# Optimization experiments

Hardware: AMD Instinct MI355X
Metric: run time of the kernel (lower is better)

Reference implementation:

```python
import jax, jax.numpy as jnp
import numpy as np

B, N, E, D, OUT, L = 4, 10000, 160000, 128, 64, 4
NEG = 0.01  # LeakyReLU slope

def lrelu(x):
    return jnp.where(x > 0, x, NEG * x)

def setup_inputs() -> dict:
    key = jax.random.key(0)
    ks = jax.random.split(key, 20)
    s = 0.05
    inp = {
        "x": jax.random.normal(ks[0], (B, N * 3), dtype=jnp.float32),
        "edge_index": jax.random.randint(ks[1], (2, E), 0, N, dtype=jnp.int32),
        # f0: Linear(3, D)
        "w0": jax.random.normal(ks[2], (3, D), dtype=jnp.float32) * s,
        "b0": jax.random.normal(ks[3], (D,), dtype=jnp.float32) * s,
        # per-layer params stacked on leading L axis
        "ew1": jax.random.normal(ks[4], (L, 2 * D + 1, D), dtype=jnp.float32) * s,
        "eb1": jax.random.normal(ks[5], (L, D), dtype=jnp.float32) * s,
        "ew2": jax.random.normal(ks[6], (L, D, D), dtype=jnp.float32) * s,
        "eb2": jax.random.normal(ks[7], (L, D), dtype=jnp.float32) * s,
        "cw": jax.random.normal(ks[8], (L, D, 1), dtype=jnp.float32) * s,
        "cb": jax.random.normal(ks[9], (L, 1), dtype=jnp.float32) * s,
        "nw1": jax.random.normal(ks[10], (L, 2 * D, D), dtype=jnp.float32) * s,
        "nb1": jax.random.normal(ks[11], (L, D), dtype=jnp.float32) * s,
        "nw2": jax.random.normal(ks[12], (L, D, D), dtype=jnp.float32) * s,
        "nb2": jax.random.normal(ks[13], (L, D), dtype=jnp.float32) * s,
        # project: Linear(D, OUT)
        "wp": jax.random.normal(ks[14], (D, OUT), dtype=jnp.float32) * s,
        "bp": jax.random.normal(ks[15], (OUT,), dtype=jnp.float32) * s,
    }
    return inp

def reference(x, edge_index, w0, b0, ew1, eb1, ew2, eb2, cw, cb, nw1, nb1, nw2, nb2, wp, bp):
    b = x.shape[0]
    n = x.shape[1] // 3
    pos = x.reshape(b, n, 3)            # coordinates [B,N,3]
    h = lrelu(pos @ w0 + b0)            # node features [B,N,D]
    row, col = edge_index[0], edge_index[1]
    # per-node in-edge counts (same for all layers/batches); scatter_mean -> 0 for empty nodes
    cnt = jnp.zeros((n,), x.dtype).at[col].add(1.0)
    denom = jnp.maximum(cnt, 1.0)[None, :, None]
    for i in range(L):
        rel = pos[:, row] - pos[:, col]                          # [B,E,3]
        dist_sq = jnp.sum(rel * rel, axis=-1, keepdims=True)     # [B,E,1]
        edge_in = jnp.concatenate([h[:, row], h[:, col], dist_sq], axis=-1)  # [B,E,2D+1]
        msg = lrelu(lrelu(edge_in @ ew1[i] + eb1[i]) @ ew2[i] + eb2[i])       # [B,E,D]
        aggr = jnp.zeros((b, n, msg.shape[-1]), msg.dtype).at[:, col].add(msg) / denom  # scatter_mean
        coord_update = jnp.tanh(aggr @ cw[i] + cb[i])            # [B,N,1]
        pos = pos + coord_update * 0.1
        node_in = jnp.concatenate([h, aggr], axis=-1)            # [B,N,2D]
        h = h + lrelu(lrelu(node_in @ nw1[i] + nb1[i]) @ nw2[i] + nb2[i])
    return lrelu(h.mean(axis=1) @ wp + bp)                       # [B,OUT]
```

## Files before the change

kernel.cpp:

```cpp
#include <hip/hip_runtime.h>
#include <hip/hip_bf16.h>
#include <math.h>

#define BB   4
#define NN   10000
#define NP   10112
#define NB16 (NP / 16)
#define EE   160000
#define DD   128
#define OUTD 64
#define LL   4
#define NEGS 0.01f
#define MSTR 136
#define RSH  68

typedef __attribute__((ext_vector_type(8))) short   short8;
typedef __attribute__((ext_vector_type(4))) float   floatx4;

__device__ __forceinline__ float lrelu(float x) { return fmaxf(x, NEGS * x); }
__device__ __forceinline__ ushort f2bf(float x) {
    uint u = __builtin_bit_cast(uint, x);
    return (ushort)((u + 0x7FFFu + ((u >> 16) & 1u)) >> 16);
}
__device__ __forceinline__ float bf2f(ushort u) {
    uint v = ((uint)u) << 16;
    return __builtin_bit_cast(float, v);
}

__global__ void k_cvtw(const float* __restrict__ src, ushort* __restrict__ dst,
                       int rowpitch, int nks) {
    int tid = blockIdx.x * 256 + threadIdx.x;
    if (tid >= LL * nks * 512) return;
    int lane = tid & 63;
    int nt   = (tid >> 6) & 7;
    int ks   = (tid >> 9) % nks;
    int l    = tid / (nks * 512);
    int quad = lane >> 4, l16 = lane & 15;
    int n = nt * 16 + l16;
    const float* s = src + (size_t)l * rowpitch * DD;
    ushort* d = dst + (size_t)tid * 8;
    #pragma unroll
    for (int j = 0; j < 8; ++j)
        d[j] = f2bf(s[(size_t)(ks * 32 + quad * 8 + j) * DD + n]);
}

__global__ void k_h0(const float* __restrict__ x, const float* __restrict__ w0,
                     const float* __restrict__ b0, float* __restrict__ hp,
                     ushort* __restrict__ hb) {
    int idx = blockIdx.x * 256 + threadIdx.x;
    if (idx >= BB * NP * DD) return;
    int tile = idx >> 11, in = idx & 2047;
    int b = tile / NB16, g16 = tile % NB16;
    int nt = in >> 8, lane = (in >> 2) & 63, r = in & 3;
    int quad = lane >> 4, l16 = lane & 15;
    int n = g16 * 16 + quad * 4 + r;
    int d = nt * 16 + l16;
    float v = 0.0f;
    if (n < NN) {
        const float* p = x + ((size_t)b * NN + n) * 3;
        v = lrelu(b0[d] + p[0] * w0[d] + p[1] * w0[DD + d] + p[2] * w0[2 * DD + d]);
    }
    hp[idx] = v;
    hb[((size_t)b * NP + n) * DD + d] = f2bf(v);
}

__global__ void k_count(const int* __restrict__ col, float* __restrict__ cnt,
                        int* __restrict__ ecnt) {
    int e = blockIdx.x * blockDim.x + threadIdx.x;
    if (e < EE) {
        int c = col[e];
        atomicAdd(&cnt[c], 1.0f);
        atomicAdd(&ecnt[c], 1);
    }
}

__global__ __launch_bounds__(256) void k_scan(const int* __restrict__ ecnt,
                                              int* __restrict__ cursor) {
    __shared__ int s_sum[256];
    int t = threadIdx.x;
    int base = t * 40;
    int s = 0;
    for (int i = 0; i < 40; ++i) {
        int n = base + i;
        if (n < NN) s += ecnt[n];
    }
    s_sum[t] = s;
    __syncthreads();
    if (t == 0) {
        int a = 0;
        for (int i = 0; i < 256; ++i) { int v = s_sum[i]; s_sum[i] = a; a += v; }
    }
    __syncthreads();
    int a = s_sum[t];
    for (int i = 0; i < 40; ++i) {
        int n = base + i;
        if (n < NN) { cursor[n] = a; a += ecnt[n]; }
    }
}

__global__ void k_place(const int* __restrict__ row, const int* __restrict__ col,
                        int* __restrict__ cursor,
                        int* __restrict__ rowS, int* __restrict__ colS) {
    int e = blockIdx.x * blockDim.x + threadIdx.x;
    if (e >= EE) return;
    int c = col[e];
    int p = atomicAdd(&cursor[c], 1);
    rowS[p] = row[e];
    colS[p] = c;
}

__global__ __launch_bounds__(256) void k_pq(
    const ushort* __restrict__ hb, const ushort* __restrict__ wtf,
    const ushort* __restrict__ wmf, const float* __restrict__ b1,
    ushort* __restrict__ P, ushort* __restrict__ Q)
{
    __shared__ __align__(16) ushort s_out[64 * MSTR];
    const int b = blockIdx.y, n0 = blockIdx.x * 64, t = threadIdx.x;
    const int w = t >> 6, lane = t & 63, quad = lane >> 4, l16 = lane & 15;
    const int rw = w * 16;
    const int nw = n0 + rw;

    const ushort* hptr = hb + ((size_t)b * NP + nw + l16) * DD;
    float b1r[8];
    #pragma unroll
    for (int nt = 0; nt < 8; ++nt) b1r[nt] = b1[nt * 16 + l16];

    const short8* wt = (const short8*)wtf;
    const short8* wm = (const short8*)wmf;

    #pragma unroll
    for (int pass = 0; pass < 2; ++pass) {
        floatx4 ap[8];
        #pragma unroll
        for (int nt = 0; nt < 8; ++nt)
            #pragma unroll
            for (int r = 0; r < 4; ++r) ap[nt][r] = pass ? b1r[nt] : 0.0f;
        const short8* wv = pass ? wm : wt;
        #pragma unroll
        for (int ks = 0; ks < 4; ++ks) {
            short8 bf[8];
            #pragma unroll
            for (int nt = 0; nt < 8; ++nt) bf[nt] = wv[(ks * 8 + nt) * 64 + lane];
            short8 af = *(const short8*)(hptr + ks * 32 + quad * 8);
            #pragma unroll
            for (int nt = 0; nt < 8; ++nt)
                ap[nt] = __builtin_amdgcn_mfma_f32_16x16x32_bf16(af, bf[nt], ap[nt], 0, 0, 0);
        }
        #pragma unroll
        for (int nt = 0; nt < 8; ++nt)
            #pragma unroll
            for (int r = 0; r < 4; ++r)
                s_out[(rw + quad * 4 + r) * MSTR + nt * 16 + l16] = f2bf(ap[nt][r]);
        ushort* dst = pass ? Q : P;
        #pragma unroll
        for (int i = 0; i < 4; ++i) {
            int row = rw + i * 4 + quad;
            short8 v = *(const short8*)&s_out[row * MSTR + l16 * 8];
            *(short8*)(dst + ((size_t)b * NP + n0 + row) * DD + l16 * 8) = v;
        }
    }
}

__global__ __launch_bounds__(256, 4) void k_edge(
    const float* __restrict__ pos,
    const ushort* __restrict__ P, const ushort* __restrict__ Q,
    const int* __restrict__ rowS, const int* __restrict__ colS,
    const float* __restrict__ w1last,
    const ushort* __restrict__ w2f, const float* __restrict__ b2,
    float* __restrict__ aggr)
{
    __shared__ int    s_row[128];
    __shared__ int    s_col[128];
    __shared__ float  s_ds[128];
    __shared__ __align__(16) ushort s_red[128 * RSH];

    const int g    = blockIdx.x;
    const int b    = (g >> 1) & 3;
    const int tile = (g >> 3) * 2 + (g & 1);
    const int e0   = tile * 128;
    const int t    = threadIdx.x;
    const int w    = t >> 6, lane = t & 63;
    const int quad = lane >> 4, l16 = lane & 15;

    if (t < 128) {
        int e = e0 + t;
        int r = rowS[e], c = colS[e];
        s_row[t] = r;
        s_col[t] = c;
        const float* pr = pos + ((size_t)b * NN + r) * 3;
        const float* pc = pos + ((size_t)b * NN + c) * 3;
        float dx = pr[0] - pc[0], dy = pr[1] - pc[1], dz = pr[2] - pc[2];
        s_ds[t] = dx * dx + dy * dy + dz * dz;
    }
    __syncthreads();

    const int ew = w * 32;
    const ushort* pp[2];
    const ushort* qp[2];
    float dsv[2];
    #pragma unroll
    for (int mt = 0; mt < 2; ++mt) {
        int el = ew + mt * 16 + l16;
        pp[mt]  = P + ((size_t)b * NP + s_row[el]) * DD;
        qp[mt]  = Q + ((size_t)b * NP + s_col[el]) * DD;
        dsv[mt] = s_ds[el];
    }

    short8 pf[2][4], qf[2][4];
    #pragma unroll
    for (int ks = 0; ks < 4; ++ks) {
        const int koff = ks * 32 + quad * 8;
        #pragma unroll
        for (int mt = 0; mt < 2; ++mt) {
            pf[mt][ks] = *(const short8*)(pp[mt] + koff);
            qf[mt][ks] = *(const short8*)(qp[mt] + koff);
        }
    }

    short8 mid[2][4];
    #pragma unroll
    for (int ks = 0; ks < 4; ++ks) {
        const int koff = ks * 32 + quad * 8;
        floatx4 wl0 = *(const floatx4*)(w1last + koff);
        floatx4 wl1 = *(const floatx4*)(w1last + koff + 4);
        #pragma unroll
        for (int mt = 0; mt < 2; ++mt) {
            #pragma unroll
            for (int j = 0; j < 4; ++j) {
                float v = bf2f((ushort)pf[mt][ks][j]) + bf2f((ushort)qf[mt][ks][j]) + dsv[mt] * wl0[j];
                mid[mt][ks][j] = (short)f2bf(lrelu(v));
            }
            #pragma unroll
            for (int j = 0; j < 4; ++j) {
                float v = bf2f((ushort)pf[mt][ks][4 + j]) + bf2f((ushort)qf[mt][ks][4 + j]) + dsv[mt] * wl1[j];
                mid[mt][ks][4 + j] = (short)f2bf(lrelu(v));
            }
        }
    }

    float b2r[8];
    #pragma unroll
    for (int nt = 0; nt < 8; ++nt) b2r[nt] = b2[nt * 16 + l16];

    const short8* w2v = (const short8*)w2f;
    #pragma unroll
    for (int ph = 0; ph < 2; ++ph) {
        floatx4 acc[2][4];
        #pragma unroll
        for (int mt = 0; mt < 2; ++mt)
            #pragma unroll
            for (int ntl = 0; ntl < 4; ++ntl)
                #pragma unroll
                for (int r = 0; r < 4; ++r) acc[mt][ntl][r] = b2r[ph * 4 + ntl];

        #pragma unroll
        for (int ks = 0; ks < 4; ++ks) {
            short8 bf[4];
            #pragma unroll
            for (int ntl = 0; ntl < 4; ++ntl)
                bf[ntl] = w2v[(ks * 8 + ph * 4 + ntl) * 64 + lane];
            #pragma unroll
            for (int mt = 0; mt < 2; ++mt)
                #pragma unroll
                for (int ntl = 0; ntl < 4; ++ntl)
                    acc[mt][ntl] = __builtin_amdgcn_mfma_f32_16x16x32_bf16(mid[mt][ks], bf[ntl], acc[mt][ntl], 0, 0, 0);
        }

        #pragma unroll
        for (int mt = 0; mt < 2; ++mt)
            #pragma unroll
            for (int ntl = 0; ntl < 4; ++ntl)
                #pragma unroll
                for (int r = 0; r < 4; ++r)
                    s_red[(ew + mt * 16 + quad * 4 + r) * RSH + ntl * 16 + l16] =
                        f2bf(lrelu(acc[mt][ntl][r]));

        const int d = ph * 64 + lane;
        float run = 0.0f;
        int prev = s_col[ew];
        for (int r = 0; r < 32; ++r) {
            int cid = s_col[ew + r];
            float v = bf2f(s_red[(ew + r) * RSH + lane]);
            if (cid != prev) {
                atomicAdd(&aggr[((size_t)b * NP + prev) * DD + d], run);
                run = 0.0f;
                prev = cid;
            }
            run += v;
        }
        atomicAdd(&aggr[((size_t)b * NP + prev) * DD + d], run);
    }
}

__global__ __launch_bounds__(256) void k_node(
    ushort* hb, float* aggr, const float* __restrict__ cnt,
    const float* __restrict__ cw, const float* __restrict__ cb,
    const ushort* __restrict__ w1f, const float* __restrict__ b1,
    const ushort* __restrict__ w2f, const float* __restrict__ b2,
    float* hp, float* __restrict__ pos,
    int do_pq,
    const ushort* __restrict__ wtn, const ushort* __restrict__ wmn,
    const float* __restrict__ b1n,
    ushort* __restrict__ P, ushort* __restrict__ Q)
{
    __shared__ __align__(16) ushort s_mid[64 * MSTR];
    __shared__ __align__(16) ushort s_out[64 * MSTR];

    const int g    = blockIdx.x;
    const int b    = (g >> 1) & 3;
    const int tile = (g >> 3) * 2 + (g & 1);
    const int n0   = tile * 64;
    const int t    = threadIdx.x;
    const int w    = t >> 6, lane = t & 63;
    const int quad = lane >> 4, l16 = lane & 15;
    const int rw   = w * 16;
    const int nw   = n0 + rw;

    const ushort* hptr = hb + ((size_t)b * NP + nw + l16) * DD;
    float* aptr = aggr + ((size_t)b * NP + nw + l16) * DD;
    float inv = 0.0f;
    {
        int node = nw + l16;
        if (node < NN) { float dn = cnt[node]; inv = 1.0f / fmaxf(dn, 1.0f); }
    }
    float b1r[8], b2r[8];
    #pragma unroll
    for (int nt = 0; nt < 8; ++nt) {
        int d = nt * 16 + l16;
        b1r[nt] = b1[d]; b2r[nt] = b2[d];
    }

    floatx4 acc[8];
    #pragma unroll
    for (int nt = 0; nt < 8; ++nt)
        #pragma unroll
        for (int r = 0; r < 4; ++r) acc[nt][r] = b1r[nt];

    float cwacc = 0.0f;
    const floatx4 zero4 = {0.0f, 0.0f, 0.0f, 0.0f};
    const short8* w1v = (const short8*)w1f;
    #pragma unroll
    for (int ks = 0; ks < 8; ++ks) {
        short8 bf[8];
        #pragma unroll
        for (int nt = 0; nt < 8; ++nt) bf[nt] = w1v[(ks * 8 + nt) * 64 + lane];
        const int koff = (ks & 3) * 32 + quad * 8;
        if (ks < 4) {
            short8 af = *(const short8*)(hptr + koff);
            #pragma unroll
            for (int nt = 0; nt < 8; ++nt)
                acc[nt] = __builtin_amdgcn_mfma_f32_16x16x32_bf16(af, bf[nt], acc[nt], 0, 0, 0);
        } else {
            floatx4 cw0 = *(const floatx4*)(cw + koff);
            floatx4 cw1 = *(const floatx4*)(cw + koff + 4);
            floatx4 a0 = *(const floatx4*)(aptr + koff);
            floatx4 a1 = *(const floatx4*)(aptr + koff + 4);
            *(floatx4*)(aptr + koff)     = zero4;
            *(floatx4*)(aptr + koff + 4) = zero4;
            short8 af;
            #pragma unroll
            for (int j = 0; j < 4; ++j) {
                float v = a0[j] * inv;
                af[j] = (short)f2bf(v);
                cwacc += v * cw0[j];
            }
            #pragma unroll
            for (int j = 0; j < 4; ++j) {
                float v = a1[j] * inv;
                af[4 + j] = (short)f2bf(v);
                cwacc += v * cw1[j];
            }
            #pragma unroll
            for (int nt = 0; nt < 8; ++nt)
                acc[nt] = __builtin_amdgcn_mfma_f32_16x16x32_bf16(af, bf[nt], acc[nt], 0, 0, 0);
        }
    }

    {
        float full = cwacc;
        full += __shfl_xor(full, 16);
        full += __shfl_xor(full, 32);
        int node = nw + l16;
        if (quad == 0 && node < NN) {
            float cu = 0.1f * tanhf(full + cb[0]);
            float* pp = pos + ((size_t)b * NN + node) * 3;
            pp[0] += cu; pp[1] += cu; pp[2] += cu;
        }
    }

    #pragma unroll
    for (int nt = 0; nt < 8; ++nt)
        #pragma unroll
        for (int r = 0; r < 4; ++r)
            s_mid[(rw + quad * 4 + r) * MSTR + nt * 16 + l16] = f2bf(lrelu(acc[nt][r]));

    const size_t hbase = ((size_t)b * NB16 + (nw >> 4)) * 2048;
    floatx4 ho[8];
    #pragma unroll
    for (int nt = 0; nt < 8; ++nt)
        ho[nt] = *(const floatx4*)(hp + hbase + nt * 256 + lane * 4);

    floatx4 acc2[8];
    #pragma unroll
    for (int nt = 0; nt < 8; ++nt)
        #pragma unroll
        for (int r = 0; r < 4; ++r) acc2[nt][r] = b2r[nt];

    const short8* w2v = (const short8*)w2f;
    #pragma unroll
    for (int ks = 0; ks < 4; ++ks) {
        short8 bf[8];
        #pragma unroll
        for (int nt = 0; nt < 8; ++nt) bf[nt] = w2v[(ks * 8 + nt) * 64 + lane];
        short8 af = *(const short8*)(&s_mid[(rw + l16) * MSTR + ks * 32 + quad * 8]);
        #pragma unroll
        for (int nt = 0; nt < 8; ++nt)
            acc2[nt] = __builtin_amdgcn_mfma_f32_16x16x32_bf16(af, bf[nt], acc2[nt], 0, 0, 0);
    }

    #pragma unroll
    for (int nt = 0; nt < 8; ++nt) {
        floatx4 hv;
        #pragma unroll
        for (int r = 0; r < 4; ++r) hv[r] = ho[nt][r] + lrelu(acc2[nt][r]);
        *(floatx4*)(hp + hbase + nt * 256 + lane * 4) = hv;
        #pragma unroll
        for (int r = 0; r < 4; ++r)
            s_mid[(rw + quad * 4 + r) * MSTR + nt * 16 + l16] = f2bf(hv[r]);
    }

    #pragma unroll
    for (int i = 0; i < 4; ++i) {
        int row = rw + i * 4 + quad;
        int n = n0 + row;
        short8 v = *(const short8*)&s_mid[row * MSTR + l16 * 8];
        if (n < NN)
            *(short8*)(hb + ((size_t)b * NP + n) * DD + l16 * 8) = v;
    }

    if (do_pq) {
        const short8* wt = (const short8*)wtn;
        const short8* wm = (const short8*)wmn;
        float b1nr[8];
        #pragma unroll
        for (int nt = 0; nt < 8; ++nt) b1nr[nt] = b1n[nt * 16 + l16];

        #pragma unroll
        for (int pass = 0; pass < 2; ++pass) {
            floatx4 ap[8];
            #pragma unroll
            for (int nt = 0; nt < 8; ++nt)
                #pragma unroll
                for (int r = 0; r < 4; ++r) ap[nt][r] = pass ? b1nr[nt] : 0.0f;
            const short8* wv = pass ? wm : wt;
            #pragma unroll
            for (int ks = 0; ks < 4; ++ks) {
                short8 bf[8];
                #pragma unroll
                for (int nt = 0; nt < 8; ++nt) bf[nt] = wv[(ks * 8 + nt) * 64 + lane];
                short8 af = *(const short8*)(&s_mid[(rw + l16) * MSTR + ks * 32 + quad * 8]);
                #pragma unroll
                for (int nt = 0; nt < 8; ++nt)
                    ap[nt] = __builtin_amdgcn_mfma_f32_16x16x32_bf16(af, bf[nt], ap[nt], 0, 0, 0);
            }
            #pragma unroll
            for (int nt = 0; nt < 8; ++nt)
                #pragma unroll
                for (int r = 0; r < 4; ++r)
                    s_out[(rw + quad * 4 + r) * MSTR + nt * 16 + l16] = f2bf(ap[nt][r]);
            ushort* dst = pass ? Q : P;
            #pragma unroll
            for (int i = 0; i < 4; ++i) {
                int row = rw + i * 4 + quad;
                short8 v = *(const short8*)&s_out[row * MSTR + l16 * 8];
                *(short8*)(dst + ((size_t)b * NP + n0 + row) * DD + l16 * 8) = v;
            }
        }
    }
}

#define NPC 50
__global__ void k_mean(const ushort* __restrict__ hb, float* __restrict__ hm) {
    int b  = blockIdx.y;
    int n0 = blockIdx.x * NPC;
    int d  = threadIdx.x;
    float s = 0.0f;
    for (int n = n0; n < n0 + NPC; ++n) s += bf2f(hb[((size_t)b * NP + n) * DD + d]);
    atomicAdd(&hm[b * DD + d], s);
}

__global__ void k_proj(const float* __restrict__ hm, const float* __restrict__ wp,
                       const float* __restrict__ bp, float* __restrict__ out) {
    int t = threadIdx.x;
    int b = t >> 6, o = t & (OUTD - 1);
    float s = 0.0f;
    for (int d2 = 0; d2 < DD; ++d2) s += hm[b * DD + d2] * wp[d2 * OUTD + o];
    s = s * (1.0f / NN) + bp[o];
    out[b * OUTD + o] = lrelu(s);
}

extern "C" void kernel_launch(void* const* d_in, const int* in_sizes, int n_in,
                              void* d_out, int out_size, void* d_ws, size_t ws_size,
                              hipStream_t stream) {
    (void)in_sizes; (void)n_in; (void)out_size; (void)ws_size;
    const float* x   = (const float*)d_in[0];
    const int*   ei  = (const int*)d_in[1];
    const float* w0  = (const float*)d_in[2];
    const float* b0  = (const float*)d_in[3];
    const float* ew1 = (const float*)d_in[4];
    const float* eb1 = (const float*)d_in[5];
    const float* ew2 = (const float*)d_in[6];
    const float* eb2 = (const float*)d_in[7];
    const float* cw  = (const float*)d_in[8];
    const float* cb  = (const float*)d_in[9];
    const float* nw1 = (const float*)d_in[10];
    const float* nb1 = (const float*)d_in[11];
    const float* nw2 = (const float*)d_in[12];
    const float* nb2 = (const float*)d_in[13];
    const float* wp  = (const float*)d_in[14];
    const float* bp  = (const float*)d_in[15];
    const int* row = ei;
    const int* col = ei + EE;

    const size_t HSZ = (size_t)BB * NP * DD;
    float* ws   = (float*)d_ws;
    float* hp   = ws;
    float* aggr = hp + HSZ;
    float* pos  = aggr + HSZ;
    float* cnt  = pos + (size_t)BB * NN * 3;
    float* hm   = cnt + NN;
    ushort* hb    = (ushort*)(hm + 512);
    ushort* Pb    = hb + HSZ;
    ushort* Qb    = Pb + HSZ;
    ushort* wtopf = Qb + HSZ;
    ushort* wmidf = wtopf + (size_t)LL * 16384;
    ushort* ew2f  = wmidf + (size_t)LL * 16384;
    ushort* nw1f  = ew2f + (size_t)LL * 16384;
    ushort* nw2f  = nw1f + (size_t)LL * 32768;
    int* ecnt   = (int*)(nw2f + (size_t)LL * 16384);
    int* cursor = ecnt + NN;
    int* rowS   = cursor + NN;
    int* colS   = rowS + EE;

    hipMemcpyAsync(pos, x, sizeof(float) * (size_t)BB * NN * 3,
                   hipMemcpyDeviceToDevice, stream);
    hipMemsetAsync(cnt, 0, sizeof(float) * NN, stream);
    hipMemsetAsync(ecnt, 0, sizeof(int) * NN, stream);
    hipMemsetAsync(hm, 0, sizeof(float) * BB * DD, stream);
    hipMemsetAsync(aggr, 0, sizeof(float) * HSZ, stream);

    k_cvtw<<<(LL * 4 * 512 + 255) / 256, 256, 0, stream>>>(ew1, wtopf, 257, 4);
    k_cvtw<<<(LL * 4 * 512 + 255) / 256, 256, 0, stream>>>(ew1 + (size_t)128 * DD, wmidf, 257, 4);
    k_cvtw<<<(LL * 4 * 512 + 255) / 256, 256, 0, stream>>>(ew2, ew2f, 128, 4);
    k_cvtw<<<(LL * 8 * 512 + 255) / 256, 256, 0, stream>>>(nw1, nw1f, 256, 8);
    k_cvtw<<<(LL * 4 * 512 + 255) / 256, 256, 0, stream>>>(nw2, nw2f, 128, 4);

    k_h0<<<((int)HSZ + 255) / 256, 256, 0, stream>>>(x, w0, b0, hp, hb);
    k_count<<<(EE + 255) / 256, 256, 0, stream>>>(col, cnt, ecnt);
    k_scan<<<1, 256, 0, stream>>>(ecnt, cursor);
    k_place<<<(EE + 255) / 256, 256, 0, stream>>>(row, col, cursor, rowS, colS);

    k_pq<<<dim3(NP / 64, BB), 256, 0, stream>>>(hb, wtopf, wmidf, eb1, Pb, Qb);

    for (int i = 0; i < LL; ++i) {
        k_edge<<<(EE / 128) * BB, 256, 0, stream>>>(
            pos, Pb, Qb, rowS, colS,
            ew1 + (size_t)i * 257 * DD + (size_t)256 * DD,
            ew2f + (size_t)i * 16384,
            eb2 + (size_t)i * DD,
            aggr);
        int nx = (i < LL - 1) ? (i + 1) : i;
        k_node<<<(NP / 64) * BB, 256, 0, stream>>>(
            hb, aggr, cnt,
            cw + (size_t)i * DD, cb + i,
            nw1f + (size_t)i * 32768, nb1 + (size_t)i * DD,
            nw2f + (size_t)i * 16384, nb2 + (size_t)i * DD,
            hp, pos,
            (i < LL - 1) ? 1 : 0,
            wtopf + (size_t)nx * 16384, wmidf + (size_t)nx * 16384,
            eb1 + (size_t)nx * DD,
            Pb, Qb);
    }

    k_mean<<<dim3(NN / NPC, BB), DD, 0, stream>>>(hb, hm);
    k_proj<<<1, 256, 0, stream>>>(hm, wp, bp, (float*)d_out);
}
```

Baseline: 613.1 us.

## Drop fp32 hidden-state buffer, merge weight conversions, stage h in LDS

Removes the fp32 residual copy of h and keeps node features only in bf16, reading the old h into shared memory once per tile and reusing it for both the first GEMM and the residual add. The five weight-conversion launches are merged into one kernel, and k_pq uses the same interleaved block-to-batch mapping as the other kernels. In the edge kernel, bf16 unpacking is done with 32-bit shift and mask ops, and the per-edge reduction buffer is kept in fp32 instead of bf16. The intent is to cut global traffic and launch count. The trade-off is that the residual now accumulates in bf16 across layers, which loses precision, and the edge kernel uses more shared memory, which could lower occupancy.

```diff
diff --git a/kernel.cpp b/kernel.cpp
--- a/kernel.cpp
+++ b/kernel.cpp
@@ -5,17 +5,17 @@
 #define BB   4
 #define NN   10000
 #define NP   10112
-#define NB16 (NP / 16)
 #define EE   160000
 #define DD   128
 #define OUTD 64
 #define LL   4
 #define NEGS 0.01f
 #define MSTR 136
-#define RSH  68
+#define RSF  68
 
 typedef __attribute__((ext_vector_type(8))) short   short8;
 typedef __attribute__((ext_vector_type(4))) float   floatx4;
+typedef __attribute__((ext_vector_type(4))) uint    uintx4;
 
 __device__ __forceinline__ float lrelu(float x) { return fmaxf(x, NEGS * x); }
 __device__ __forceinline__ ushort f2bf(float x) {
@@ -26,42 +26,46 @@
     uint v = ((uint)u) << 16;
     return __builtin_bit_cast(float, v);
 }
-
-__global__ void k_cvtw(const float* __restrict__ src, ushort* __restrict__ dst,
-                       int rowpitch, int nks) {
+__device__ __forceinline__ float bcf(uint u) { return __builtin_bit_cast(float, u); }
+
+__global__ void k_cvtw_all(const float* __restrict__ ew1, const float* __restrict__ ew2,
+                           const float* __restrict__ nw1, const float* __restrict__ nw2,
+                           ushort* __restrict__ wtopf, ushort* __restrict__ wmidf,
+                           ushort* __restrict__ ew2f, ushort* __restrict__ nw1f,
+                           ushort* __restrict__ nw2f) {
     int tid = blockIdx.x * 256 + threadIdx.x;
-    if (tid >= LL * nks * 512) return;
-    int lane = tid & 63;
-    int nt   = (tid >> 6) & 7;
-    int ks   = (tid >> 9) % nks;
-    int l    = tid / (nks * 512);
+    const float* src; ushort* dst; int pitch, nks, loc;
+    if (tid < 8192)       { src = ew1;                     dst = wtopf; pitch = 257; nks = 4; loc = tid; }
+    else if (tid < 16384) { src = ew1 + (size_t)128 * DD;  dst = wmidf; pitch = 257; nks = 4; loc = tid - 8192; }
+    else if (tid < 24576) { src = ew2;                     dst = ew2f;  pitch = 128; nks = 4; loc = tid - 16384; }
+    else if (tid < 40960) { src = nw1;                     dst = nw1f;  pitch = 256; nks = 8; loc = tid - 24576; }
+    else                  { src = nw2;                     dst = nw2f;  pitch = 128; nks = 4; loc = tid - 40960; }
+    int lane = loc & 63;
+    int nt   = (loc >> 6) & 7;
+    int ks   = (loc >> 9) % nks;
+    int l    = loc / (nks * 512);
     int quad = lane >> 4, l16 = lane & 15;
     int n = nt * 16 + l16;
-    const float* s = src + (size_t)l * rowpitch * DD;
-    ushort* d = dst + (size_t)tid * 8;
+    const float* s = src + (size_t)l * pitch * DD;
+    ushort* d = dst + (size_t)loc * 8;
     #pragma unroll
     for (int j = 0; j < 8; ++j)
         d[j] = f2bf(s[(size_t)(ks * 32 + quad * 8 + j) * DD + n]);
 }
 
 __global__ void k_h0(const float* __restrict__ x, const float* __restrict__ w0,
-                     const float* __restrict__ b0, float* __restrict__ hp,
-                     ushort* __restrict__ hb) {
+                     const float* __restrict__ b0, ushort* __restrict__ hb) {
     int idx = blockIdx.x * 256 + threadIdx.x;
     if (idx >= BB * NP * DD) return;
-    int tile = idx >> 11, in = idx & 2047;
-    int b = tile / NB16, g16 = tile % NB16;
-    int nt = in >> 8, lane = (in >> 2) & 63, r = in & 3;
-    int quad = lane >> 4, l16 = lane & 15;
-    int n = g16 * 16 + quad * 4 + r;
-    int d = nt * 16 + l16;
+    int d  = idx & (DD - 1);
+    int bn = idx >> 7;
+    int n  = bn % NP, b = bn / NP;
     float v = 0.0f;
     if (n < NN) {
         const float* p = x + ((size_t)b * NN + n) * 3;
         v = lrelu(b0[d] + p[0] * w0[d] + p[1] * w0[DD + d] + p[2] * w0[2 * DD + d]);
     }
-    hp[idx] = v;
-    hb[((size_t)b * NP + n) * DD + d] = f2bf(v);
+    hb[idx] = f2bf(v);
 }
 
 __global__ void k_count(const int* __restrict__ col, float* __restrict__ cnt,
@@ -115,7 +119,10 @@
     ushort* __restrict__ P, ushort* __restrict__ Q)
 {
     __shared__ __align__(16) ushort s_out[64 * MSTR];
-    const int b = blockIdx.y, n0 = blockIdx.x * 64, t = threadIdx.x;
+    const int g = blockIdx.x;
+    const int b = (g >> 1) & 3;
+    const int n0 = ((g >> 3) * 2 + (g & 1)) * 64;
+    const int t = threadIdx.x;
     const int w = t >> 6, lane = t & 63, quad = lane >> 4, l16 = lane & 15;
     const int rw = w * 16;
     const int nw = n0 + rw;
@@ -172,7 +179,7 @@
     __shared__ int    s_row[128];
     __shared__ int    s_col[128];
     __shared__ float  s_ds[128];
-    __shared__ __align__(16) ushort s_red[128 * RSH];
+    __shared__ float  s_red[128 * RSF];
 
     const int g    = blockIdx.x;
     const int b    = (g >> 1) & 3;
@@ -206,34 +213,33 @@
         dsv[mt] = s_ds[el];
     }
 
-    short8 pf[2][4], qf[2][4];
+    uintx4 pf[2][4], qf[2][4];
     #pragma unroll
     for (int ks = 0; ks < 4; ++ks) {
         const int koff = ks * 32 + quad * 8;
         #pragma unroll
         for (int mt = 0; mt < 2; ++mt) {
-            pf[mt][ks] = *(const short8*)(pp[mt] + koff);
-            qf[mt][ks] = *(const short8*)(qp[mt] + koff);
-        }
-    }
-
-    short8 mid[2][4];
+            pf[mt][ks] = *(const uintx4*)(pp[mt] + koff);
+            qf[mt][ks] = *(const uintx4*)(qp[mt] + koff);
+        }
+    }
+
+    uintx4 mid[2][4];
     #pragma unroll
     for (int ks = 0; ks < 4; ++ks) {
         const int koff = ks * 32 + quad * 8;
         floatx4 wl0 = *(const floatx4*)(w1last + koff);
         floatx4 wl1 = *(const floatx4*)(w1last + koff + 4);
+        float wl[8] = {wl0[0], wl0[1], wl0[2], wl0[3], wl1[0], wl1[1], wl1[2], wl1[3]};
         #pragma unroll
         for (int mt = 0; mt < 2; ++mt) {
             #pragma unroll
-            for (int j = 0; j < 4; ++j) {
-                float v = bf2f((ushort)pf[mt][ks][j]) + bf2f((ushort)qf[mt][ks][j]) + dsv[mt] * wl0[j];
-                mid[mt][ks][j] = (short)f2bf(lrelu(v));
-            }
-            #pragma unroll
-            for (int j = 0; j < 4; ++j) {
-                float v = bf2f((ushort)pf[mt][ks][4 + j]) + bf2f((ushort)qf[mt][ks][4 + j]) + dsv[mt] * wl1[j];
-                mid[mt][ks][4 + j] = (short)f2bf(lrelu(v));
+            for (int i = 0; i < 4; ++i) {
+                uint pv = pf[mt][ks][i], qv = qf[mt][ks][i];
+                float vlo = lrelu(bcf(pv << 16) + bcf(qv << 16) + dsv[mt] * wl[2 * i]);
+                float vhi = lrelu(bcf(pv & 0xFFFF0000u) + bcf(qv & 0xFFFF0000u) + dsv[mt] * wl[2 * i + 1]);
+                mid[mt][ks][i] = (__builtin_bit_cast(uint, vlo) >> 16) |
+                                 (__builtin_bit_cast(uint, vhi) & 0xFFFF0000u);
             }
         }
     }
@@ -260,10 +266,12 @@
             for (int ntl = 0; ntl < 4; ++ntl)
                 bf[ntl] = w2v[(ks * 8 + ph * 4 + ntl) * 64 + lane];
             #pragma unroll
-            for (int mt = 0; mt < 2; ++mt)
+            for (int mt = 0; mt < 2; ++mt) {
+                short8 af = __builtin_bit_cast(short8, mid[mt][ks]);
                 #pragma unroll
                 for (int ntl = 0; ntl < 4; ++ntl)
-                    acc[mt][ntl] = __builtin_amdgcn_mfma_f32_16x16x32_bf16(mid[mt][ks], bf[ntl], acc[mt][ntl], 0, 0, 0);
+                    acc[mt][ntl] = __builtin_amdgcn_mfma_f32_16x16x32_bf16(af, bf[ntl], acc[mt][ntl], 0, 0, 0);
+            }
         }
 
         #pragma unroll
@@ -272,15 +280,15 @@
             for (int ntl = 0; ntl < 4; ++ntl)
                 #pragma unroll
                 for (int r = 0; r < 4; ++r)
-                    s_red[(ew + mt * 16 + quad * 4 + r) * RSH + ntl * 16 + l16] =
-                        f2bf(lrelu(acc[mt][ntl][r]));
+                    s_red[(ew + mt * 16 + quad * 4 + r) * RSF + ntl * 16 + l16] =
+                        lrelu(acc[mt][ntl][r]);
 
         const int d = ph * 64 + lane;
         float run = 0.0f;
         int prev = s_col[ew];
         for (int r = 0; r < 32; ++r) {
             int cid = s_col[ew + r];
-            float v = bf2f(s_red[(ew + r) * RSH + lane]);
+            float v = s_red[(ew + r) * RSF + lane];
             if (cid != prev) {
                 atomicAdd(&aggr[((size_t)b * NP + prev) * DD + d], run);
                 run = 0.0f;
@@ -297,26 +305,31 @@
     const float* __restrict__ cw, const float* __restrict__ cb,
     const ushort* __restrict__ w1f, const float* __restrict__ b1,
     const ushort* __restrict__ w2f, const float* __restrict__ b2,
-    float* hp, float* __restrict__ pos,
+    float* __restrict__ pos,
     int do_pq,
     const ushort* __restrict__ wtn, const ushort* __restrict__ wmn,
     const float* __restrict__ b1n,
     ushort* __restrict__ P, ushort* __restrict__ Q)
 {
     __shared__ __align__(16) ushort s_mid[64 * MSTR];
-    __shared__ __align__(16) ushort s_out[64 * MSTR];
+    __shared__ __align__(16) ushort s_ho[64 * MSTR];
 
     const int g    = blockIdx.x;
     const int b    = (g >> 1) & 3;
-    const int tile = (g >> 3) * 2 + (g & 1);
-    const int n0   = tile * 64;
+    const int n0   = ((g >> 3) * 2 + (g & 1)) * 64;
     const int t    = threadIdx.x;
     const int w    = t >> 6, lane = t & 63;
     const int quad = lane >> 4, l16 = lane & 15;
     const int rw   = w * 16;
     const int nw   = n0 + rw;
 
-    const ushort* hptr = hb + ((size_t)b * NP + nw + l16) * DD;
+    #pragma unroll
+    for (int i = 0; i < 4; ++i) {
+        int row = rw + i * 4 + quad;
+        short8 v = *(const short8*)(hb + ((size_t)b * NP + n0 + row) * DD + l16 * 8);
+        *(short8*)&s_ho[row * MSTR + l16 * 8] = v;
+    }
+
     float* aptr = aggr + ((size_t)b * NP + nw + l16) * DD;
     float inv = 0.0f;
     {
@@ -346,7 +359,7 @@
         for (int nt = 0; nt < 8; ++nt) bf[nt] = w1v[(ks * 8 + nt) * 64 + lane];
         const int koff = (ks & 3) * 32 + quad * 8;
         if (ks < 4) {
-            short8 af = *(const short8*)(hptr + koff);
+            short8 af = *(const short8*)(&s_ho[(rw + l16) * MSTR + koff]);
             #pragma unroll
             for (int nt = 0; nt < 8; ++nt)
                 acc[nt] = __builtin_amdgcn_mfma_f32_16x16x32_bf16(af, bf[nt], acc[nt], 0, 0, 0);
@@ -394,12 +407,6 @@
         for (int r = 0; r < 4; ++r)
             s_mid[(rw + quad * 4 + r) * MSTR + nt * 16 + l16] = f2bf(lrelu(acc[nt][r]));
 
-    const size_t hbase = ((size_t)b * NB16 + (nw >> 4)) * 2048;
-    floatx4 ho[8];
-    #pragma unroll
-    for (int nt = 0; nt < 8; ++nt)
-        ho[nt] = *(const floatx4*)(hp + hbase + nt * 256 + lane * 4);
-
     floatx4 acc2[8];
     #pragma unroll
     for (int nt = 0; nt < 8; ++nt)
@@ -419,15 +426,14 @@
     }
 
     #pragma unroll
-    for (int nt = 0; nt < 8; ++nt) {
-        floatx4 hv;
-        #pragma unroll
-        for (int r = 0; r < 4; ++r) hv[r] = ho[nt][r] + lrelu(acc2[nt][r]);
-        *(floatx4*)(hp + hbase + nt * 256 + lane * 4) = hv;
-        #pragma unroll
-        for (int r = 0; r < 4; ++r)
-            s_mid[(rw + quad * 4 + r) * MSTR + nt * 16 + l16] = f2bf(hv[r]);
-    }
+    for (int nt = 0; nt < 8; ++nt)
+        #pragma unroll
+        for (int r = 0; r < 4; ++r) {
+            int row = rw + quad * 4 + r;
+            float hold = bf2f(s_ho[row * MSTR + nt * 16 + l16]);
+            float hv = hold + lrelu(acc2[nt][r]);
+            s_mid[row * MSTR + nt * 16 + l16] = f2bf(hv);
+        }
 
     #pragma unroll
     for (int i = 0; i < 4; ++i) {
@@ -467,12 +473,12 @@
             for (int nt = 0; nt < 8; ++nt)
                 #pragma unroll
                 for (int r = 0; r < 4; ++r)
-                    s_out[(rw + quad * 4 + r) * MSTR + nt * 16 + l16] = f2bf(ap[nt][r]);
+                    s_ho[(rw + quad * 4 + r) * MSTR + nt * 16 + l16] = f2bf(ap[nt][r]);
             ushort* dst = pass ? Q : P;
             #pragma unroll
             for (int i = 0; i < 4; ++i) {
                 int row = rw + i * 4 + quad;
-                short8 v = *(const short8*)&s_out[row * MSTR + l16 * 8];
+                short8 v = *(const short8*)&s_ho[row * MSTR + l16 * 8];
                 *(short8*)(dst + ((size_t)b * NP + n0 + row) * DD + l16 * 8) = v;
             }
         }
@@ -524,8 +530,7 @@
 
     const size_t HSZ = (size_t)BB * NP * DD;
     float* ws   = (float*)d_ws;
-    float* hp   = ws;
-    float* aggr = hp + HSZ;
+    float* aggr = ws;
     float* pos  = aggr + HSZ;
     float* cnt  = pos + (size_t)BB * NN * 3;
     float* hm   = cnt + NN;
@@ -549,18 +554,15 @@
     hipMemsetAsync(hm, 0, sizeof(float) * BB * DD, stream);
     hipMemsetAsync(aggr, 0, sizeof(float) * HSZ, stream);
 
-    k_cvtw<<<(LL * 4 * 512 + 255) / 256, 256, 0, stream>>>(ew1, wtopf, 257, 4);
-    k_cvtw<<<(LL * 4 * 512 + 255) / 256, 256, 0, stream>>>(ew1 + (size_t)128 * DD, wmidf, 257, 4);
-    k_cvtw<<<(LL * 4 * 512 + 255) / 256, 256, 0, stream>>>(ew2, ew2f, 128, 4);
-    k_cvtw<<<(LL * 8 * 512 + 255) / 256, 256, 0, stream>>>(nw1, nw1f, 256, 8);
-    k_cvtw<<<(LL * 4 * 512 + 255) / 256, 256, 0, stream>>>(nw2, nw2f, 128, 4);
-
-    k_h0<<<((int)HSZ + 255) / 256, 256, 0, stream>>>(x, w0, b0, hp, hb);
+    k_cvtw_all<<<192, 256, 0, stream>>>(ew1, ew2, nw1, nw2,
+                                        wtopf, wmidf, ew2f, nw1f, nw2f);
+
+    k_h0<<<((int)HSZ + 255) / 256, 256, 0, stream>>>(x, w0, b0, hb);
     k_count<<<(EE + 255) / 256, 256, 0, stream>>>(col, cnt, ecnt);
     k_scan<<<1, 256, 0, stream>>>(ecnt, cursor);
     k_place<<<(EE + 255) / 256, 256, 0, stream>>>(row, col, cursor, rowS, colS);
 
-    k_pq<<<dim3(NP / 64, BB), 256, 0, stream>>>(hb, wtopf, wmidf, eb1, Pb, Qb);
+    k_pq<<<(NP / 64) * BB, 256, 0, stream>>>(hb, wtopf, wmidf, eb1, Pb, Qb);
 
     for (int i = 0; i < LL; ++i) {
         k_edge<<<(EE / 128) * BB, 256, 0, stream>>>(
@@ -575,7 +577,7 @@
             cw + (size_t)i * DD, cb + i,
             nw1f + (size_t)i * 32768, nb1 + (size_t)i * DD,
             nw2f + (size_t)i * 16384, nb2 + (size_t)i * DD,
-            hp, pos,
+            pos,
             (i < LL - 1) ? 1 : 0,
             wtopf + (size_t)nx * 16384, wmidf + (size_t)nx * 16384,
             eb1 + (size_t)nx * DD,
```

After: 593.6 us, median of 3. 3.2% less time.
